# Kernel tuning notes

Hardware: AMD Instinct MI355X
Metric: run time of the kernel (lower is better)

Reference implementation:

```python
import jax, jax.numpy as jnp
import numpy as np

D_PRIME = 512
D = 2048
CLASSES = 4


def setup_inputs() -> dict:
    key = jax.random.key(0)
    k1, k2, k3, k4 = jax.random.split(key, 4)
    N = 32768
    V_prime = jax.random.normal(k1, (N, D), dtype=jnp.float32)
    U_t = jax.random.normal(k2, (D_PRIME, D), dtype=jnp.float32)
    W_mta = jax.random.normal(k3, (1, D_PRIME), dtype=jnp.float32)
    W = jax.random.normal(k4, (CLASSES, D), dtype=jnp.float32)
    return {"V_prime": V_prime, "U_t": U_t, "W_mta": W_mta, "W": W}


def reference(V_prime, U_t, W_mta, W):
    # [D_prime, N] = tanh(U_t @ V'^T)
    tanh_scores = jnp.tanh(U_t @ V_prime.T)
    # attention over instances: [1, N]
    a = jax.nn.softmax(W_mta @ tanh_scores, axis=1)
    # weighted sum pooling: [D]
    t = jnp.sum(a.T * V_prime, axis=0)
    # final linear: [1, classes]
    l = (W @ t).reshape(1, CLASSES)
    return l
```

## Files before the change

kernel.cpp:

```cpp
#include <hip/hip_runtime.h>

#define N_INST 32768
#define DIM    2048
#define DP     512
#define NCLS   4

typedef _Float16 half8_t __attribute__((ext_vector_type(8)));
typedef float    float4_t __attribute__((ext_vector_type(4)));

#define OFF_UHI   0ull
#define OFF_S     (OFF_UHI  + (size_t)DP*DIM*2)
#define OFF_STAT  (OFF_S    + (size_t)N_INST*4)
#define OFF_PSTAT (OFF_STAT + 256ull)
#define OFF_PART  (OFF_PSTAT+ 256ull)

__device__ __forceinline__ float tanh_fast(float x) {
  float e = __expf(2.0f * x);
  return 1.0f - 2.0f / (e + 1.0f);
}

__global__ __launch_bounds__(256) void k_cvt(const float4* __restrict__ in,
                                             half8_t* __restrict__ out) {
  int i = blockIdx.x * 256 + threadIdx.x;
  float4 a = in[2 * i], b = in[2 * i + 1];
  half8_t h;
  h[0] = (_Float16)a.x; h[1] = (_Float16)a.y;
  h[2] = (_Float16)a.z; h[3] = (_Float16)a.w;
  h[4] = (_Float16)b.x; h[5] = (_Float16)b.y;
  h[6] = (_Float16)b.z; h[7] = (_Float16)b.w;
  out[i] = h;
}

__global__ __launch_bounds__(256) void k_score_gemm(
    const _Float16* __restrict__ Uhi, const float* __restrict__ V,
    const float* __restrict__ Wmta, float* __restrict__ s) {
  __shared__ _Float16 lA[128 * 32];
  __shared__ _Float16 lB[128 * 32];

  const int tid = threadIdx.x;
  const int lane = tid & 63;
  const int wv = tid >> 6;
  const int waveM = wv >> 1;
  const int waveN = wv & 1;
  const int quad = lane >> 4;
  const int col = lane & 15;

  const int b = blockIdx.x;
  const int grp = b >> 5;
  const int win = b & 31;
  const int mb = win >> 3;
  const int nb = grp * 8 + (win & 7);

  const int aRow0 = mb * 128;
  const int bRow0 = nb * 128;
  const int kStart = (nb & 63) << 5;

  float4_t acc[4][4];
  const float4_t z4 = {0.f, 0.f, 0.f, 0.f};
  for (int i = 0; i < 4; i++)
    for (int j = 0; j < 4; j++) acc[i][j] = z4;

  const int stR = tid >> 2;
  const int stQ = (tid & 3) << 3;

  const _Float16* gA0 = Uhi + (size_t)(aRow0 + stR) * DIM + stQ;
  const _Float16* gA1 = Uhi + (size_t)(aRow0 + 64 + stR) * DIM + stQ;
  const float*    gB0 = V   + (size_t)(bRow0 + stR) * DIM + stQ;
  const float*    gB1 = V   + (size_t)(bRow0 + 64 + stR) * DIM + stQ;

  uint4  ra0, ra1;
  float4 rb0a, rb0b, rb1a, rb1b;

  ra0 = *(const uint4*)(gA0 + kStart);  ra1 = *(const uint4*)(gA1 + kStart);
  rb0a = *(const float4*)(gB0 + kStart);  rb0b = *(const float4*)(gB0 + kStart + 4);
  rb1a = *(const float4*)(gB1 + kStart);  rb1b = *(const float4*)(gB1 + kStart + 4);

  for (int ki = 0; ki < 64; ++ki) {
    __syncthreads();
    *(uint4*)&lA[stR * 32 + stQ] = ra0;
    *(uint4*)&lA[(stR + 64) * 32 + stQ] = ra1;
    {
      half8_t h0, h1;
      h0[0] = (_Float16)rb0a.x; h0[1] = (_Float16)rb0a.y;
      h0[2] = (_Float16)rb0a.z; h0[3] = (_Float16)rb0a.w;
      h0[4] = (_Float16)rb0b.x; h0[5] = (_Float16)rb0b.y;
      h0[6] = (_Float16)rb0b.z; h0[7] = (_Float16)rb0b.w;
      h1[0] = (_Float16)rb1a.x; h1[1] = (_Float16)rb1a.y;
      h1[2] = (_Float16)rb1a.z; h1[3] = (_Float16)rb1a.w;
      h1[4] = (_Float16)rb1b.x; h1[5] = (_Float16)rb1b.y;
      h1[6] = (_Float16)rb1b.z; h1[7] = (_Float16)rb1b.w;
      *(half8_t*)&lB[stR * 32 + stQ] = h0;
      *(half8_t*)&lB[(stR + 64) * 32 + stQ] = h1;
    }
    __syncthreads();

    const int kp = (kStart + (ki + 1) * 32) & (DIM - 1);
    ra0 = *(const uint4*)(gA0 + kp);  ra1 = *(const uint4*)(gA1 + kp);
    rb0a = *(const float4*)(gB0 + kp);  rb0b = *(const float4*)(gB0 + kp + 4);
    rb1a = *(const float4*)(gB1 + kp);  rb1b = *(const float4*)(gB1 + kp + 4);

    half8_t af[4], bf[4];
    for (int mi = 0; mi < 4; mi++) {
      const int row = waveM * 64 + mi * 16 + col;
      af[mi] = *(const half8_t*)&lA[row * 32 + quad * 8];
    }
    for (int ni = 0; ni < 4; ni++) {
      const int row = waveN * 64 + ni * 16 + col;
      bf[ni] = *(const half8_t*)&lB[row * 32 + quad * 8];
    }
    for (int mi = 0; mi < 4; mi++)
      for (int ni = 0; ni < 4; ni++)
        acc[mi][ni] = __builtin_amdgcn_mfma_f32_16x16x32_f16(af[mi], bf[ni], acc[mi][ni], 0, 0, 0);
  }

  for (int ni = 0; ni < 4; ni++) {
    float v = 0.0f;
    for (int mi = 0; mi < 4; mi++) {
      const int jb = aRow0 + waveM * 64 + mi * 16 + quad * 4;
      union { float4_t v4; float f[4]; } u;
      u.v4 = acc[mi][ni];
      for (int r = 0; r < 4; r++)
        v += Wmta[jb + r] * tanh_fast(u.f[r]);
    }
    v += __shfl_xor(v, 16);
    v += __shfl_xor(v, 32);
    if (quad == 0) {
      const int n = bRow0 + waveN * 64 + ni * 16 + col;
      atomicAdd(&s[n], v);
    }
  }
}

__global__ __launch_bounds__(256) void k_stats1(const float* __restrict__ s,
                                                float* __restrict__ pstat) {
  const int tid = threadIdx.x;
  const int lane = tid & 63;
  const int wvi = tid >> 6;
  __shared__ float smM[4], smP[4];
  const float4* s4 = (const float4*)s;

  float4 v = s4[blockIdx.x * 256 + tid];
  float m = fmaxf(fmaxf(v.x, v.y), fmaxf(v.z, v.w));
  float p = __expf(v.x - m) + __expf(v.y - m) + __expf(v.z - m) + __expf(v.w - m);
  for (int o = 32; o > 0; o >>= 1) {
    float om = __shfl_xor(m, o);
    float op = __shfl_xor(p, o);
    float nm = fmaxf(m, om);
    p = p * __expf(m - nm) + op * __expf(om - nm);
    m = nm;
  }
  if (lane == 0) { smM[wvi] = m; smP[wvi] = p; }
  __syncthreads();
  if (tid == 0) {
    float gm = fmaxf(fmaxf(smM[0], smM[1]), fmaxf(smM[2], smM[3]));
    float sum = 0.f;
    for (int w = 0; w < 4; w++) sum += smP[w] * __expf(smM[w] - gm);
    pstat[blockIdx.x * 2]     = gm;
    pstat[blockIdx.x * 2 + 1] = sum;
  }
}

__global__ __launch_bounds__(64) void k_stats2(const float* __restrict__ pstat,
                                               float* __restrict__ stats) {
  const int tid = threadIdx.x;
  float m = -3.4e38f, p = 0.0f;
  if (tid < 32) { m = pstat[tid * 2]; p = pstat[tid * 2 + 1]; }
  for (int o = 32; o > 0; o >>= 1) {
    float om = __shfl_xor(m, o);
    float op = __shfl_xor(p, o);
    float nm = fmaxf(m, om);
    p = p * __expf(m - nm) + op * __expf(om - nm);
    m = nm;
  }
  if (tid == 0) { stats[0] = m; stats[1] = 1.0f / p; }
}

__global__ __launch_bounds__(256) void k_pool(const float* __restrict__ V,
                                              const float* __restrict__ s,
                                              const float* __restrict__ stats,
                                              float* __restrict__ part) {
  const int tid = threadIdx.x;
  const float mx = stats[0], inv = stats[1];
  const int n0 = blockIdx.x * 128;
  float acc[8] = {0.f, 0.f, 0.f, 0.f, 0.f, 0.f, 0.f, 0.f};
  for (int r = 0; r < 128; ++r) {
    const int n = n0 + r;
    const float w = __expf(s[n] - mx) * inv;
    if (w > 1e-12f) {
      const float4* vp = (const float4*)&V[(size_t)n * DIM + tid * 8];
      float4 va = vp[0], vb = vp[1];
      acc[0] += w * va.x; acc[1] += w * va.y; acc[2] += w * va.z; acc[3] += w * va.w;
      acc[4] += w * vb.x; acc[5] += w * vb.y; acc[6] += w * vb.z; acc[7] += w * vb.w;
    }
  }
  float* dst = &part[(size_t)blockIdx.x * DIM + tid * 8];
  *(float4*)(dst + 0) = make_float4(acc[0], acc[1], acc[2], acc[3]);
  *(float4*)(dst + 4) = make_float4(acc[4], acc[5], acc[6], acc[7]);
}

__global__ __launch_bounds__(256) void k_reduce_final(const float* __restrict__ part,
                                                      const float* __restrict__ W,
                                                      float* __restrict__ out) {
  const int d = blockIdx.x * 256 + threadIdx.x;
  float t = 0.f;
  for (int bb = 0; bb < 256; ++bb) t += part[(size_t)bb * DIM + d];

  float pc[NCLS];
#pragma unroll
  for (int c = 0; c < NCLS; ++c) pc[c] = W[(size_t)c * DIM + d] * t;

  __shared__ float sred[4][NCLS];
  const int lane = threadIdx.x & 63;
  const int wvi = threadIdx.x >> 6;
#pragma unroll
  for (int c = 0; c < NCLS; ++c)
    for (int o = 32; o > 0; o >>= 1) pc[c] += __shfl_xor(pc[c], o);
  if (lane == 0)
    for (int c = 0; c < NCLS; ++c) sred[wvi][c] = pc[c];
  __syncthreads();
  if (threadIdx.x < NCLS) {
    float v = sred[0][threadIdx.x] + sred[1][threadIdx.x] +
              sred[2][threadIdx.x] + sred[3][threadIdx.x];
    atomicAdd(&out[threadIdx.x], v);
  }
}

extern "C" void kernel_launch(void* const* d_in, const int* in_sizes, int n_in,
                              void* d_out, int out_size, void* d_ws, size_t ws_size,
                              hipStream_t stream) {
  const float* Vp   = (const float*)d_in[0];
  const float* Ut   = (const float*)d_in[1];
  const float* Wmta = (const float*)d_in[2];
  const float* W    = (const float*)d_in[3];
  float* out = (float*)d_out;

  char* ws = (char*)d_ws;
  _Float16* Uhi  = (_Float16*)(ws + OFF_UHI);
  float*    sBuf = (float*)(ws + OFF_S);
  float*    stat = (float*)(ws + OFF_STAT);
  float*    pstat= (float*)(ws + OFF_PSTAT);
  float*    partB= (float*)(ws + OFF_PART);

  hipMemsetAsync(sBuf, 0, (size_t)N_INST * 4, stream);
  hipMemsetAsync(out, 0, (size_t)NCLS * 4, stream);

  k_cvt<<<(DP * DIM / 8) / 256, 256, 0, stream>>>((const float4*)Ut, (half8_t*)Uhi);
  k_score_gemm<<<(DP / 128) * (N_INST / 128), 256, 0, stream>>>(Uhi, Vp, Wmta, sBuf);
  k_stats1<<<32, 256, 0, stream>>>(sBuf, pstat);
  k_stats2<<<1, 64, 0, stream>>>(pstat, stat);
  k_pool<<<N_INST / 128, 256, 0, stream>>>(Vp, sBuf, stat, partB);
  k_reduce_final<<<DIM / 256, 256, 0, stream>>>(partB, W, out);
}
```

Baseline: 490.4 us.

## Pre-convert V to fp16 and double-buffer GEMM tiles via direct global-to-LDS loads

Adds a conversion pass that turns V' into fp16 in the workspace, so the score GEMM reads half-width data and no longer converts in the inner loop. The GEMM now fetches A and B tiles with global_load_lds straight into shared memory, using two LDS buffers so the next k-slice loads while the current one feeds the MFMAs, with one barrier per iteration instead of two. It also raises the occupancy hint in launch_bounds and drops the staggered k start. In exchange, the conversion pass reads the full fp32 V' and writes a 128 MB fp16 copy, which adds memory traffic ahead of the GEMM.

```diff
diff --git a/kernel.cpp b/kernel.cpp
--- a/kernel.cpp
+++ b/kernel.cpp
@@ -8,11 +8,16 @@
 typedef _Float16 half8_t __attribute__((ext_vector_type(8)));
 typedef float    float4_t __attribute__((ext_vector_type(4)));
 
-#define OFF_UHI   0ull
+#define OFF_VHI   0ull
+#define OFF_UHI   (OFF_VHI  + (size_t)N_INST*DIM*2)
 #define OFF_S     (OFF_UHI  + (size_t)DP*DIM*2)
 #define OFF_STAT  (OFF_S    + (size_t)N_INST*4)
 #define OFF_PSTAT (OFF_STAT + 256ull)
 #define OFF_PART  (OFF_PSTAT+ 256ull)
+
+#define GLOAD_LDS16(g, l) __builtin_amdgcn_global_load_lds( \
+    (__attribute__((address_space(1))) void*)(g),           \
+    (__attribute__((address_space(3))) void*)(l), 16, 0, 0)
 
 __device__ __forceinline__ float tanh_fast(float x) {
   float e = __expf(2.0f * x);
@@ -31,11 +36,11 @@
   out[i] = h;
 }
 
-__global__ __launch_bounds__(256) void k_score_gemm(
-    const _Float16* __restrict__ Uhi, const float* __restrict__ V,
+__global__ __launch_bounds__(256, 4) void k_score_gemm(
+    const _Float16* __restrict__ Uhi, const _Float16* __restrict__ Vhi,
     const float* __restrict__ Wmta, float* __restrict__ s) {
-  __shared__ _Float16 lA[128 * 32];
-  __shared__ _Float16 lB[128 * 32];
+  __shared__ _Float16 lA[2][128 * 32];
+  __shared__ _Float16 lB[2][128 * 32];
 
   const int tid = threadIdx.x;
   const int lane = tid & 63;
@@ -53,7 +58,6 @@
 
   const int aRow0 = mb * 128;
   const int bRow0 = nb * 128;
-  const int kStart = (nb & 63) << 5;
 
   float4_t acc[4][4];
   const float4_t z4 = {0.f, 0.f, 0.f, 0.f};
@@ -61,52 +65,40 @@
     for (int j = 0; j < 4; j++) acc[i][j] = z4;
 
   const int stR = tid >> 2;
-  const int stQ = (tid & 3) << 3;
-
-  const _Float16* gA0 = Uhi + (size_t)(aRow0 + stR) * DIM + stQ;
-  const _Float16* gA1 = Uhi + (size_t)(aRow0 + 64 + stR) * DIM + stQ;
-  const float*    gB0 = V   + (size_t)(bRow0 + stR) * DIM + stQ;
-  const float*    gB1 = V   + (size_t)(bRow0 + 64 + stR) * DIM + stQ;
-
-  uint4  ra0, ra1;
-  float4 rb0a, rb0b, rb1a, rb1b;
-
-  ra0 = *(const uint4*)(gA0 + kStart);  ra1 = *(const uint4*)(gA1 + kStart);
-  rb0a = *(const float4*)(gB0 + kStart);  rb0b = *(const float4*)(gB0 + kStart + 4);
-  rb1a = *(const float4*)(gB1 + kStart);  rb1b = *(const float4*)(gB1 + kStart + 4);
+  const int stC = (tid & 3) << 3;
+
+  const _Float16* gA0 = Uhi + (size_t)(aRow0 + stR) * DIM + stC;
+  const _Float16* gA1 = Uhi + (size_t)(aRow0 + 64 + stR) * DIM + stC;
+  const _Float16* gB0 = Vhi + (size_t)(bRow0 + stR) * DIM + stC;
+  const _Float16* gB1 = Vhi + (size_t)(bRow0 + 64 + stR) * DIM + stC;
+  const int lbase0 = (wv << 6) << 3;
+  const int lbase1 = (256 + (wv << 6)) << 3;
+
+  GLOAD_LDS16(gA0, &lA[0][lbase0]);
+  GLOAD_LDS16(gA1, &lA[0][lbase1]);
+  GLOAD_LDS16(gB0, &lB[0][lbase0]);
+  GLOAD_LDS16(gB1, &lB[0][lbase1]);
 
   for (int ki = 0; ki < 64; ++ki) {
+    const int cur = ki & 1, nxt = cur ^ 1;
     __syncthreads();
-    *(uint4*)&lA[stR * 32 + stQ] = ra0;
-    *(uint4*)&lA[(stR + 64) * 32 + stQ] = ra1;
-    {
-      half8_t h0, h1;
-      h0[0] = (_Float16)rb0a.x; h0[1] = (_Float16)rb0a.y;
-      h0[2] = (_Float16)rb0a.z; h0[3] = (_Float16)rb0a.w;
-      h0[4] = (_Float16)rb0b.x; h0[5] = (_Float16)rb0b.y;
-      h0[6] = (_Float16)rb0b.z; h0[7] = (_Float16)rb0b.w;
-      h1[0] = (_Float16)rb1a.x; h1[1] = (_Float16)rb1a.y;
-      h1[2] = (_Float16)rb1a.z; h1[3] = (_Float16)rb1a.w;
-      h1[4] = (_Float16)rb1b.x; h1[5] = (_Float16)rb1b.y;
-      h1[6] = (_Float16)rb1b.z; h1[7] = (_Float16)rb1b.w;
-      *(half8_t*)&lB[stR * 32 + stQ] = h0;
-      *(half8_t*)&lB[(stR + 64) * 32 + stQ] = h1;
-    }
-    __syncthreads();
-
-    const int kp = (kStart + (ki + 1) * 32) & (DIM - 1);
-    ra0 = *(const uint4*)(gA0 + kp);  ra1 = *(const uint4*)(gA1 + kp);
-    rb0a = *(const float4*)(gB0 + kp);  rb0b = *(const float4*)(gB0 + kp + 4);
-    rb1a = *(const float4*)(gB1 + kp);  rb1b = *(const float4*)(gB1 + kp + 4);
+
+    if (ki + 1 < 64) {
+      const int kn = (ki + 1) << 5;
+      GLOAD_LDS16(gA0 + kn, &lA[nxt][lbase0]);
+      GLOAD_LDS16(gA1 + kn, &lA[nxt][lbase1]);
+      GLOAD_LDS16(gB0 + kn, &lB[nxt][lbase0]);
+      GLOAD_LDS16(gB1 + kn, &lB[nxt][lbase1]);
+    }
 
     half8_t af[4], bf[4];
     for (int mi = 0; mi < 4; mi++) {
       const int row = waveM * 64 + mi * 16 + col;
-      af[mi] = *(const half8_t*)&lA[row * 32 + quad * 8];
+      af[mi] = *(const half8_t*)&lA[cur][row * 32 + quad * 8];
     }
     for (int ni = 0; ni < 4; ni++) {
       const int row = waveN * 64 + ni * 16 + col;
-      bf[ni] = *(const half8_t*)&lB[row * 32 + quad * 8];
+      bf[ni] = *(const half8_t*)&lB[cur][row * 32 + quad * 8];
     }
     for (int mi = 0; mi < 4; mi++)
       for (int ni = 0; ni < 4; ni++)
@@ -235,6 +227,7 @@
   float* out = (float*)d_out;
 
   char* ws = (char*)d_ws;
+  _Float16* Vhi  = (_Float16*)(ws + OFF_VHI);
   _Float16* Uhi  = (_Float16*)(ws + OFF_UHI);
   float*    sBuf = (float*)(ws + OFF_S);
   float*    stat = (float*)(ws + OFF_STAT);
@@ -244,8 +237,9 @@
   hipMemsetAsync(sBuf, 0, (size_t)N_INST * 4, stream);
   hipMemsetAsync(out, 0, (size_t)NCLS * 4, stream);
 
+  k_cvt<<<(N_INST * DIM / 8) / 256, 256, 0, stream>>>((const float4*)Vp, (half8_t*)Vhi);
   k_cvt<<<(DP * DIM / 8) / 256, 256, 0, stream>>>((const float4*)Ut, (half8_t*)Uhi);
-  k_score_gemm<<<(DP / 128) * (N_INST / 128), 256, 0, stream>>>(Uhi, Vp, Wmta, sBuf);
+  k_score_gemm<<<(DP / 128) * (N_INST / 128), 256, 0, stream>>>(Uhi, Vhi, Wmta, sBuf);
   k_stats1<<<32, 256, 0, stream>>>(sBuf, pstat);
   k_stats2<<<1, 64, 0, stream>>>(pstat, stat);
   k_pool<<<N_INST / 128, 256, 0, stream>>>(Vp, sBuf, stat, partB);
```

New measurement: 494.0 us. Within noise of the previous version (+0.7%).
